# Optimization experiments

Hardware: AMD Instinct MI355X
Metric: run time of the kernel (lower is better)

## Reference

```python
import jax, jax.numpy as jnp
import numpy as np

N_NODES = 50000
N_EDGES = 1600000
N_CAND = 1000
N_GRAPHS = 50
EMB = 32
EDGE_DIM = 1
L = 4
EPS = 1e-5


def setup_inputs() -> dict:
    key = jax.random.key(0)
    ks = jax.random.split(key, 24)
    x = jax.random.normal(ks[0], (N_NODES, 2), dtype=jnp.float32)
    edge_index = jax.random.randint(ks[1], (2, N_EDGES), 0, N_NODES)
    edge_attr = jax.random.normal(ks[2], (N_EDGES, EDGE_DIM), dtype=jnp.float32)
    candidate_idxs = jax.random.randint(ks[3], (N_CAND,), 0, N_NODES)
    batch = jnp.sort(jax.random.randint(ks[4], (N_NODES,), 0, N_GRAPHS))
    s = 0.1
    W_in = jax.random.normal(ks[5], (2, EMB), dtype=jnp.float32) * s
    b_in = jax.random.normal(ks[6], (EMB,), dtype=jnp.float32) * s
    # stacked per-layer MLP params: Linear(65->32), BN, ReLU, Linear(32->32), BN, ReLU
    W1 = jax.random.normal(ks[7], (L, 2 * EMB + EDGE_DIM, EMB), dtype=jnp.float32) * s
    b1 = jax.random.normal(ks[8], (L, EMB), dtype=jnp.float32) * s
    g1 = 1.0 + 0.1 * jax.random.normal(ks[9], (L, EMB), dtype=jnp.float32)
    be1 = 0.1 * jax.random.normal(ks[10], (L, EMB), dtype=jnp.float32)
    m1 = 0.1 * jax.random.normal(ks[11], (L, EMB), dtype=jnp.float32)
    v1 = 0.5 + jax.random.uniform(ks[12], (L, EMB), dtype=jnp.float32)
    W2 = jax.random.normal(ks[13], (L, EMB, EMB), dtype=jnp.float32) * s
    b2 = jax.random.normal(ks[14], (L, EMB), dtype=jnp.float32) * s
    g2 = 1.0 + 0.1 * jax.random.normal(ks[15], (L, EMB), dtype=jnp.float32)
    be2 = 0.1 * jax.random.normal(ks[16], (L, EMB), dtype=jnp.float32)
    m2 = 0.1 * jax.random.normal(ks[17], (L, EMB), dtype=jnp.float32)
    v2 = 0.5 + jax.random.uniform(ks[18], (L, EMB), dtype=jnp.float32)
    W_out = jax.random.normal(ks[19], (EMB, 1), dtype=jnp.float32) * s
    b_out = jax.random.normal(ks[20], (1,), dtype=jnp.float32) * s
    return dict(x=x, edge_index=edge_index, edge_attr=edge_attr,
                candidate_idxs=candidate_idxs, batch=batch,
                W_in=W_in, b_in=b_in, W1=W1, b1=b1, g1=g1, be1=be1, m1=m1, v1=v1,
                W2=W2, b2=b2, g2=g2, be2=be2, m2=m2, v2=v2, W_out=W_out, b_out=b_out)


def _bn(h, g, b, m, v):
    # eval-mode BatchNorm1d
    return (h - m) * (g * jax.lax.rsqrt(v + EPS)) + b


def _forward(x, edge_index, edge_attr, candidate_idxs, batch,
             W_in, b_in, W1, b1, g1, be1, m1, v1,
             W2, b2, g2, be2, m2, v2, W_out, b_out):
    src = edge_index[0]  # x_j
    dst = edge_index[1]  # x_i (aggregation target)
    h = x @ W_in + b_in  # [N, EMB]

    def layer(h, p):
        (w1, bb1, gg1, bbe1, mm1, vv1, w2, bb2, gg2, bbe2, mm2, vv2) = p
        msg = jnp.concatenate([h[dst], h[src], edge_attr], axis=-1)  # [E, 2*EMB+edge_dim]
        t = jax.nn.relu(_bn(msg @ w1 + bb1, gg1, bbe1, mm1, vv1))
        t = jax.nn.relu(_bn(t @ w2 + bb2, gg2, bbe2, mm2, vv2))
        agg = jax.ops.segment_sum(t, dst, num_segments=N_NODES)
        return h + agg, None

    h, _ = jax.lax.scan(layer, h, (W1, b1, g1, be1, m1, v1, W2, b2, g2, be2, m2, v2))

    logits = (h[candidate_idxs] @ W_out + b_out).squeeze(-1)  # [C]
    seg = batch[candidate_idxs]
    seg_max = jax.ops.segment_max(logits, seg, num_segments=N_GRAPHS)
    z = logits - seg_max[seg]
    lse = jnp.log(jax.ops.segment_sum(jnp.exp(z), seg, num_segments=N_GRAPHS))
    return z - lse[seg]


def reference(x, edge_index, edge_attr, candidate_idxs, batch,
              W_in, b_in, W1, b1, g1, be1, m1, v1,
              W2, b2, g2, be2, m2, v2, W_out, b_out):
    return _forward(x, edge_index, edge_attr, candidate_idxs, batch,
                    W_in, b_in, W1, b1, g1, be1, m1, v1,
                    W2, b2, g2, be2, m2, v2, W_out, b_out)
```

## Files before the change

kernel.cpp:

```cpp
#include <hip/hip_runtime.h>
#include <hip/hip_bf16.h>

#define N_NODES 50000
#define N_EDGES 1600000
#define N_CAND  1000
#define N_GRAPHS 50
#define EMB 32
#define L_LAYERS 4

#define BSH 8
#define BNODES 256
#define NBK ((N_NODES + BNODES - 1) >> BSH)
#define STILE 2048
#define NBLK_S ((N_EDGES + STILE - 1) / STILE)

#define NPW 8

#define W1A_OFF 0
#define W1B_OFF 4096
#define W2_OFF  8192
#define WE_OFF  12288
#define C1_OFF  12416
#define C2_OFF  12544
#define W2H_OFF  12672
#define WEH_OFF  14720
#define W1AH_OFF 14784
#define W1BH_OFF 16832
#define H_OFF    18880
#define NODE_F  (N_NODES * EMB)

#define BH_OFF    (H_OFF + 4 * NODE_F)
#define BOFF_OFF  (BH_OFF + NBK)
#define OFFS_OFF  (BOFF_OFF + NBK + 1)
#define CSR_OFF   (OFFS_OFF + N_NODES + 1)
#define T_OFF     (CSR_OFF + N_EDGES)

typedef float f32x4 __attribute__((ext_vector_type(4)));
typedef _Float16 f16x8 __attribute__((ext_vector_type(8)));

union HU { unsigned short u; _Float16 f; };
static __device__ __forceinline__ _Float16 h16(unsigned short u) { HU c; c.u = u; return c.f; }
static __device__ __forceinline__ unsigned short u16(_Float16 f) { HU c; c.f = f; return c.u; }

__global__ void prep_k(const float* __restrict__ W1, const float* __restrict__ b1,
                       const float* __restrict__ g1, const float* __restrict__ be1,
                       const float* __restrict__ m1, const float* __restrict__ v1,
                       const float* __restrict__ W2, const float* __restrict__ b2,
                       const float* __restrict__ g2, const float* __restrict__ be2,
                       const float* __restrict__ m2, const float* __restrict__ v2,
                       float* __restrict__ ws) {
    int t = threadIdx.x;
    _Float16* W2H  = (_Float16*)(ws + W2H_OFF);
    _Float16* WEH  = (_Float16*)(ws + WEH_OFF);
    _Float16* W1AH = (_Float16*)(ws + W1AH_OFF);
    _Float16* W1BH = (_Float16*)(ws + W1BH_OFF);
    for (int l = 0; l < L_LAYERS; ++l) {
        for (int i = t; i < 1024; i += 256) {
            int k = i >> 5, j = i & 31;
            float s1 = g1[l * 32 + j] * rsqrtf(v1[l * 32 + j] + 1e-5f);
            float s2 = g2[l * 32 + j] * rsqrtf(v2[l * 32 + j] + 1e-5f);
            float wa = W1[(l * 65 + k) * 32 + j] * s1;
            float wb = W1[(l * 65 + 32 + k) * 32 + j] * s1;
            ws[W1A_OFF + l * 1024 + i] = wa;
            ws[W1B_OFF + l * 1024 + i] = wb;
            W1AH[l * 1024 + i] = (_Float16)wa;
            W1BH[l * 1024 + i] = (_Float16)wb;
            float w2v = W2[(l * 32 + k) * 32 + j] * s2;
            ws[W2_OFF + l * 1024 + i] = w2v;
            W2H[l * 1024 + i] = (_Float16)w2v;
            if (k == 0) {
                float wev = W1[(l * 65 + 64) * 32 + j] * s1;
                ws[WE_OFF + l * 32 + j] = wev;
                WEH[l * 32 + j] = (_Float16)wev;
                ws[C1_OFF + l * 32 + j] = b1[l * 32 + j] * s1 + be1[l * 32 + j] - m1[l * 32 + j] * s1;
                ws[C2_OFF + l * 32 + j] = b2[l * 32 + j] * s2 + be2[l * 32 + j] - m2[l * 32 + j] * s2;
            }
        }
    }
}

__global__ void embed_node_k(const float* __restrict__ x, const float* __restrict__ Win,
                             const float* __restrict__ bin, const float* __restrict__ ws,
                             float* __restrict__ h, _Float16* __restrict__ hA,
                             _Float16* __restrict__ hB) {
    __shared__ float sA[1024], sB[1024];
    for (int i = threadIdx.x; i < 1024; i += blockDim.x) {
        sA[i] = ws[W1A_OFF + i];
        sB[i] = ws[W1B_OFF + i];
    }
    __syncthreads();
    int t = blockIdx.x * blockDim.x + threadIdx.x;
    if (t >= NODE_F) return;
    int n = t >> 5, j = t & 31;
    float hv = x[2 * n] * Win[j] + x[2 * n + 1] * Win[32 + j] + bin[j];
    h[t] = hv;
    float a = ws[C1_OFF + j];
    float b = 0.f;
#pragma unroll
    for (int k = 0; k < 32; ++k) {
        float hk = __shfl(hv, k, 32);
        a += hk * sA[k * 32 + j];
        b += hk * sB[k * 32 + j];
    }
    hA[t] = (_Float16)a;
    hB[t] = (_Float16)b;
}

__global__ void zero_k(int* __restrict__ p, int n) {
    int t = blockIdx.x * blockDim.x + threadIdx.x;
    if (t < n) p[t] = 0;
}

__global__ void bhist_k(const int* __restrict__ ei, int* __restrict__ bh, int* __restrict__ T) {
    __shared__ int lh[NBK];
    for (int i = threadIdx.x; i < NBK; i += 512) lh[i] = 0;
    __syncthreads();
    int tb = blockIdx.x * STILE;
#pragma unroll
    for (int i = 0; i < STILE / 512; ++i) {
        int e = tb + i * 512 + threadIdx.x;
        if (e < N_EDGES) atomicAdd(&lh[ei[N_EDGES + e] >> BSH], 1);
    }
    __syncthreads();
    for (int i = threadIdx.x; i < NBK; i += 512) {
        int c = lh[i];
        T[i * NBLK_S + blockIdx.x] = c;
        if (c) atomicAdd(&bh[i], c);
    }
}

__global__ void bscan_k(const int* __restrict__ bh, int* __restrict__ boffs) {
    __shared__ int part[1024];
    int t = threadIdx.x;
    int s = (t < NBK) ? bh[t] : 0;
    part[t] = s;
    __syncthreads();
    for (int d = 1; d < 1024; d <<= 1) {
        int v = (t >= d) ? part[t - d] : 0;
        __syncthreads();
        part[t] += v;
        __syncthreads();
    }
    if (t < NBK) boffs[t] = part[t] - s;
    if (t == 1023) boffs[NBK] = N_EDGES;
}

__global__ void bcursor_k(const int* __restrict__ boffs, int* __restrict__ T) {
    __shared__ int part[1024];
    int k = blockIdx.x, t = threadIdx.x;
    int v = (t < NBLK_S) ? T[k * NBLK_S + t] : 0;
    part[t] = v;
    __syncthreads();
    for (int d = 1; d < 1024; d <<= 1) {
        int u = (t >= d) ? part[t - d] : 0;
        __syncthreads();
        part[t] += u;
        __syncthreads();
    }
    if (t < NBLK_S) T[k * NBLK_S + t] = boffs[k] + part[t] - v;
}

__global__ void bscatter_k(const int* __restrict__ ei, const float* __restrict__ ea,
                           const int* __restrict__ T, int* __restrict__ stage_e,
                           unsigned char* __restrict__ stage_d) {
    __shared__ int lofs[NBK];
    for (int i = threadIdx.x; i < NBK; i += 512)
        lofs[i] = T[i * NBLK_S + blockIdx.x];
    __syncthreads();
    int tb = blockIdx.x * STILE;
#pragma unroll
    for (int i = 0; i < STILE / 512; ++i) {
        int e = tb + i * 512 + threadIdx.x;
        if (e < N_EDGES) {
            int src = ei[e], dst = ei[N_EDGES + e];
            int bk = dst >> BSH;
            int pos = atomicAdd(&lofs[bk], 1);
            unsigned short eh = u16((_Float16)ea[e]);
            stage_e[pos] = src | ((int)eh << 16);
            stage_d[pos] = (unsigned char)(dst & (BNODES - 1));
        }
    }
}

__global__ void bsort2_k(const int* __restrict__ boffs, const int* __restrict__ stage_e,
                         const unsigned char* __restrict__ stage_d,
                         int* __restrict__ offs, int* __restrict__ csr) {
    __shared__ int cnt[BNODES];
    __shared__ int pre[BNODES];
    __shared__ int cur[BNODES];
    const int b = blockIdx.x;
    const int nbase = b << BSH;
    const int t = threadIdx.x;
    const int beg = boffs[b], end = boffs[b + 1];
    if (t < BNODES) cnt[t] = 0;
    __syncthreads();
    for (int i = beg + t; i < end; i += 512)
        atomicAdd(&cnt[stage_d[i]], 1);
    __syncthreads();
    if (t < 64) {
        int b4 = t * 4;
        int c0 = cnt[b4], c1 = cnt[b4 + 1], c2 = cnt[b4 + 2], c3 = cnt[b4 + 3];
        int s = c0 + c1 + c2 + c3;
        int run = s;
#pragma unroll
        for (int d = 1; d < 64; d <<= 1) {
            int v = __shfl_up(run, d, 64);
            if (t >= d) run += v;
        }
        int ex = run - s;
        pre[b4] = ex; pre[b4 + 1] = ex + c0; pre[b4 + 2] = ex + c0 + c1; pre[b4 + 3] = ex + c0 + c1 + c2;
    }
    __syncthreads();
    if (t < BNODES) {
        cur[t] = pre[t];
        int n = nbase + t;
        if (n < N_NODES) offs[n] = beg + pre[t];
    }
    if (b == NBK - 1 && t == 0) offs[N_NODES] = N_EDGES;
    __syncthreads();
    for (int i = beg + t; i < end; i += 512) {
        int dloc = stage_d[i];
        int pos = beg + atomicAdd(&cur[dloc], 1);
        csr[pos] = stage_e[i];
    }
}

__launch_bounds__(256, 4)
__global__ void edge_mfma_k(const int* __restrict__ offs, const int* __restrict__ csr,
                            const float* __restrict__ ws, int l,
                            const float* __restrict__ h, const _Float16* __restrict__ hA,
                            const _Float16* __restrict__ hB, float* __restrict__ hnext,
                            _Float16* __restrict__ hAout, _Float16* __restrict__ hBout,
                            int doNext) {
    __shared__ float vbuf[4 * 256];
    const int lane = threadIdx.x & 63;
    const int wid = (blockIdx.x * 256 + threadIdx.x) >> 6;
    const int r = lane & 15;
    const int q = lane >> 4;
    const int ll = lane & 31;
    float* vb = vbuf + (threadIdx.x >> 6) * 256;
    const int nbase = wid * NPW;
    if (nbase >= N_NODES) return;

    int o[NPW + 1];
#pragma unroll
    for (int i = 0; i <= NPW; ++i)
        o[i] = __builtin_amdgcn_readfirstlane(offs[nbase + i]);

    const _Float16* W2H = (const _Float16*)(ws + W2H_OFF);
    f16x8 b0, b1;
#pragma unroll
    for (int i = 0; i < 8; ++i) {
        b0[i] = W2H[l * 1024 + (8 * q + i) * 32 + r];
        b1[i] = W2H[l * 1024 + (8 * q + i) * 32 + 16 + r];
    }
    const float c2a = ws[C2_OFF + l * 32 + r];
    const float c2b = ws[C2_OFF + l * 32 + 16 + r];
    const f32x4 zc0 = {c2a, c2a, c2a, c2a};
    const f32x4 zc1 = {c2b, c2b, c2b, c2b};
    const f16x8 we = *(const f16x8*)((const _Float16*)(ws + WEH_OFF) + l * 32 + 8 * q);
    const f16x8 zero8 = {};

#define CEI(EB, LIM) ({ int _e = (EB) + r; _e = (_e < (LIM)) ? _e : (LIM); _e = (_e > 0) ? _e : 0; _e; })

    int lim[NPW];
#pragma unroll
    for (int s = 0; s < NPW; ++s) {
        int e1 = o[s + 1] - 1;
        lim[s] = (e1 > 0) ? e1 : 0;
    }
    int pc[NPW], pn[NPW];
#pragma unroll
    for (int s = 0; s < NPW; ++s) pc[s] = csr[CEI(o[s], lim[s])];
    f16x8 hc[NPW];
#pragma unroll
    for (int s = 0; s < NPW; ++s)
        hc[s] = *(const f16x8*)(hB + (pc[s] & 0xFFFF) * 32 + 8 * q);
#pragma unroll
    for (int s = 0; s < NPW; ++s) pn[s] = csr[CEI(o[s] + 16, lim[s])];

#pragma unroll
    for (int p = 0; p < 4; ++p) {
        const int s0 = 2 * p, s1 = 2 * p + 1;
        const int n0 = nbase + s0;
        const int n1 = n0 + 1;
        const int o0 = o[s0], o1 = o[s1], o2 = o[s1 + 1];

        const f16x8 hA0 = *(const f16x8*)(hA + n0 * 32 + 8 * q);
        const f16x8 hA1 = *(const f16x8*)(hA + n1 * 32 + 8 * q);

        float ns00 = 0.f, ns01 = 0.f, ns10 = 0.f, ns11 = 0.f;
        int nit = (o1 - o0 + 15) >> 4;
        int nit1 = (o2 - o1 + 15) >> 4;
        if (nit1 > nit) nit = nit1;

        if (nit > 0) {
            const int lim0 = lim[s0], lim1 = lim[s1];
            int eb0 = o0, eb1 = o1;
            int pc0 = pc[s0], pc1 = pc[s1];
            f16x8 hc0 = hc[s0], hc1 = hc[s1];
            int pn0 = pn[s0], pn1 = pn[s1];
            for (int it = 0; it < nit; ++it) {
                f16x8 hn0 = *(const f16x8*)(hB + (pn0 & 0xFFFF) * 32 + 8 * q);
                f16x8 hn1 = *(const f16x8*)(hB + (pn1 & 0xFFFF) * 32 + 8 * q);
                int pm0 = csr[CEI(eb0 + 32, lim0)];
                int pm1 = csr[CEI(eb1 + 32, lim1)];
                _Float16 eah0 = h16((unsigned short)((unsigned)pc0 >> 16));
                _Float16 eah1 = h16((unsigned short)((unsigned)pc1 >> 16));
                f16x8 a0 = __builtin_elementwise_max(we * eah0 + (hA0 + hc0), zero8);
                f16x8 a1 = __builtin_elementwise_max(we * eah1 + (hA1 + hc1), zero8);
                f32x4 acc00 = __builtin_amdgcn_mfma_f32_16x16x32_f16(a0, b0, zc0, 0, 0, 0);
                f32x4 acc01 = __builtin_amdgcn_mfma_f32_16x16x32_f16(a0, b1, zc1, 0, 0, 0);
                f32x4 acc10 = __builtin_amdgcn_mfma_f32_16x16x32_f16(a1, b0, zc0, 0, 0, 0);
                f32x4 acc11 = __builtin_amdgcn_mfma_f32_16x16x32_f16(a1, b1, zc1, 0, 0, 0);
                int nr0 = o1 - eb0;
                int nr1 = o2 - eb1;
#pragma unroll
                for (int reg = 0; reg < 4; ++reg) {
                    int row = 4 * q + reg;
                    float m0 = (row < nr0) ? 1.f : 0.f;
                    float m1 = (row < nr1) ? 1.f : 0.f;
                    ns00 = fmaf(m0, fmaxf(acc00[reg], 0.f), ns00);
                    ns01 = fmaf(m0, fmaxf(acc01[reg], 0.f), ns01);
                    ns10 = fmaf(m1, fmaxf(acc10[reg], 0.f), ns10);
                    ns11 = fmaf(m1, fmaxf(acc11[reg], 0.f), ns11);
                }
                eb0 += 16; eb1 += 16;
                pc0 = pn0; pc1 = pn1;
                hc0 = hn0; hc1 = hn1;
                pn0 = pm0; pn1 = pm1;
            }
        }
        ns00 += __shfl_xor(ns00, 16, 64);
        ns00 += __shfl_xor(ns00, 32, 64);
        ns01 += __shfl_xor(ns01, 16, 64);
        ns01 += __shfl_xor(ns01, 32, 64);
        ns10 += __shfl_xor(ns10, 16, 64);
        ns10 += __shfl_xor(ns10, 32, 64);
        ns11 += __shfl_xor(ns11, 16, 64);
        ns11 += __shfl_xor(ns11, 32, 64);

        float v;
        if (lane < 32) {
            v = h[n0 * 32 + ll] + ((ll & 16) ? ns01 : ns00);
            hnext[n0 * 32 + ll] = v;
        } else {
            v = h[n1 * 32 + ll] + ((ll & 16) ? ns11 : ns10);
            hnext[n1 * 32 + ll] = v;
        }
        int node8 = s0 + (lane >> 5);
        vb[node8 * 32 + (ll ^ (node8 << 2))] = v;
    }
#undef CEI

    if (doNext) {
        const int lw = l + 1;
        f16x8 av;
#pragma unroll
        for (int i = 0; i < 8; ++i) {
            int rr = r & 7;
            int ch = 8 * q + i;
            float vv = vb[rr * 32 + (ch ^ (rr << 2))];
            av[i] = (r < 8) ? (_Float16)vv : (_Float16)0.f;
        }
        const _Float16* W1AH = (const _Float16*)(ws + W1AH_OFF) + lw * 1024;
        const _Float16* W1BH = (const _Float16*)(ws + W1BH_OFF) + lw * 1024;
        f16x8 wa0, wa1, wb0, wb1;
#pragma unroll
        for (int i = 0; i < 8; ++i) {
            wa0[i] = W1AH[(8 * q + i) * 32 + r];
            wa1[i] = W1AH[(8 * q + i) * 32 + 16 + r];
            wb0[i] = W1BH[(8 * q + i) * 32 + r];
            wb1[i] = W1BH[(8 * q + i) * 32 + 16 + r];
        }
        const float c1a = ws[C1_OFF + lw * 32 + r];
        const float c1b = ws[C1_OFF + lw * 32 + 16 + r];
        const f32x4 ca = {c1a, c1a, c1a, c1a};
        const f32x4 cb = {c1b, c1b, c1b, c1b};
        const f32x4 z4 = {0.f, 0.f, 0.f, 0.f};
        f32x4 dA0 = __builtin_amdgcn_mfma_f32_16x16x32_f16(av, wa0, ca, 0, 0, 0);
        f32x4 dA1 = __builtin_amdgcn_mfma_f32_16x16x32_f16(av, wa1, cb, 0, 0, 0);
        f32x4 dB0 = __builtin_amdgcn_mfma_f32_16x16x32_f16(av, wb0, z4, 0, 0, 0);
        f32x4 dB1 = __builtin_amdgcn_mfma_f32_16x16x32_f16(av, wb1, z4, 0, 0, 0);
#pragma unroll
        for (int reg = 0; reg < 4; ++reg) {
            int row = 4 * q + reg;
            int n = nbase + row;
            if (row < 8 && n < N_NODES) {
                hAout[n * 32 + r]      = (_Float16)dA0[reg];
                hAout[n * 32 + 16 + r] = (_Float16)dA1[reg];
                hBout[n * 32 + r]      = (_Float16)dB0[reg];
                hBout[n * 32 + 16 + r] = (_Float16)dB1[reg];
            }
        }
    }
}

__global__ void head_k(const float* __restrict__ h, const int* __restrict__ cand,
                       const int* __restrict__ batch, const float* __restrict__ Wout,
                       const float* __restrict__ bout, float* __restrict__ out) {
    __shared__ float Lg[N_CAND];
    __shared__ int Sg[N_CAND];
    __shared__ float gm[N_GRAPHS], gs[N_GRAPHS];
    int t = threadIdx.x;
    if (t < N_CAND) {
        int c = cand[t];
        float acc = bout[0];
#pragma unroll
        for (int j = 0; j < 32; ++j) acc += h[c * 32 + j] * Wout[j];
        Lg[t] = acc;
        Sg[t] = batch[c];
    }
    __syncthreads();
    if (t < 16 * N_GRAPHS) {
        int g = t >> 4, s = t & 15;
        float m = -1e30f;
        for (int i = s; i < N_CAND; i += 16)
            if (Sg[i] == g) m = fmaxf(m, Lg[i]);
#pragma unroll
        for (int d = 1; d < 16; d <<= 1) m = fmaxf(m, __shfl_xor(m, d, 64));
        float ssum = 0.f;
        for (int i = s; i < N_CAND; i += 16)
            if (Sg[i] == g) ssum += expf(Lg[i] - m);
#pragma unroll
        for (int d = 1; d < 16; d <<= 1) ssum += __shfl_xor(ssum, d, 64);
        if (s == 0) { gm[g] = m; gs[g] = logf(ssum); }
    }
    __syncthreads();
    if (t < N_CAND) out[t] = Lg[t] - gm[Sg[t]] - gs[Sg[t]];
}

extern "C" void kernel_launch(void* const* d_in, const int* in_sizes, int n_in,
                              void* d_out, int out_size, void* d_ws, size_t ws_size,
                              hipStream_t stream) {
    const float* x    = (const float*)d_in[0];
    const int*   ei   = (const int*)d_in[1];
    const float* eatt = (const float*)d_in[2];
    const int*   cand = (const int*)d_in[3];
    const int*   batch= (const int*)d_in[4];
    const float* Win  = (const float*)d_in[5];
    const float* bin  = (const float*)d_in[6];
    const float* W1   = (const float*)d_in[7];
    const float* b1   = (const float*)d_in[8];
    const float* g1   = (const float*)d_in[9];
    const float* be1  = (const float*)d_in[10];
    const float* m1   = (const float*)d_in[11];
    const float* v1   = (const float*)d_in[12];
    const float* W2   = (const float*)d_in[13];
    const float* b2   = (const float*)d_in[14];
    const float* g2   = (const float*)d_in[15];
    const float* be2  = (const float*)d_in[16];
    const float* m2   = (const float*)d_in[17];
    const float* v2   = (const float*)d_in[18];
    const float* Wout = (const float*)d_in[19];
    const float* bout = (const float*)d_in[20];
    float* out = (float*)d_out;
    float* ws = (float*)d_ws;

    float* h0 = ws + H_OFF;
    float* h1 = ws + H_OFF + NODE_F;
    _Float16* hA0 = (_Float16*)(ws + H_OFF + 2 * NODE_F);
    _Float16* hB0 = (_Float16*)(ws + H_OFF + 2 * NODE_F + NODE_F / 2);
    _Float16* hA1 = (_Float16*)(ws + H_OFF + 3 * NODE_F);
    _Float16* hB1 = (_Float16*)(ws + H_OFF + 3 * NODE_F + NODE_F / 2);
    int* bh    = (int*)(ws + BH_OFF);
    int* boffs = (int*)(ws + BOFF_OFF);
    int* offs  = (int*)(ws + OFFS_OFF);
    int* csr   = (int*)(ws + CSR_OFF);
    int* T     = (int*)(ws + T_OFF);
    int* stage_e = (int*)(ws + H_OFF + NODE_F);
    unsigned char* stage_d = (unsigned char*)(ws + H_OFF + 2 * NODE_F);

    prep_k<<<1, 256, 0, stream>>>(W1, b1, g1, be1, m1, v1, W2, b2, g2, be2, m2, v2, ws);

    zero_k<<<(NBK + 255) / 256, 256, 0, stream>>>(bh, NBK);
    bhist_k<<<NBLK_S, 512, 0, stream>>>(ei, bh, T);
    bscan_k<<<1, 1024, 0, stream>>>(bh, boffs);
    bcursor_k<<<NBK, 1024, 0, stream>>>(boffs, T);
    bscatter_k<<<NBLK_S, 512, 0, stream>>>(ei, eatt, T, stage_e, stage_d);
    bsort2_k<<<NBK, 512, 0, stream>>>(boffs, stage_e, stage_d, offs, csr);

    embed_node_k<<<(NODE_F + 1023) / 1024, 1024, 0, stream>>>(x, Win, bin, ws, h0, hA0, hB0);

    const int waves = (N_NODES + NPW - 1) / NPW;
    const int eblocks = (waves + 3) / 4;
    float* cur = h0;
    float* nxt = h1;
    _Float16 *cA = hA0, *cB = hB0, *nA = hA1, *nB = hB1;
    for (int l = 0; l < L_LAYERS; ++l) {
        edge_mfma_k<<<eblocks, 256, 0, stream>>>(offs, csr, ws, l, cur, cA, cB,
                                                 nxt, nA, nB, l < L_LAYERS - 1);
        float* tf = cur; cur = nxt; nxt = tf;
        _Float16* t1 = cA; cA = nA; nA = t1;
        _Float16* t2 = cB; cB = nB; nB = t2;
    }

    head_k<<<1, 1024, 0, stream>>>(cur, cand, batch, Wout, bout, out);
}
```

Measured before the change: 242.4 us.

## Halve nodes per wave, shuffle-based next-layer staging, pack sort stage into int2

```diff
diff --git a/kernel.cpp b/kernel.cpp
--- a/kernel.cpp
+++ b/kernel.cpp
@@ -14,7 +14,7 @@
 #define STILE 2048
 #define NBLK_S ((N_EDGES + STILE - 1) / STILE)
 
-#define NPW 8
+#define NPW 4
 
 #define W1A_OFF 0
 #define W1B_OFF 4096
@@ -161,8 +161,7 @@
 }
 
 __global__ void bscatter_k(const int* __restrict__ ei, const float* __restrict__ ea,
-                           const int* __restrict__ T, int* __restrict__ stage_e,
-                           unsigned char* __restrict__ stage_d) {
+                           const int* __restrict__ T, int2* __restrict__ stage) {
     __shared__ int lofs[NBK];
     for (int i = threadIdx.x; i < NBK; i += 512)
         lofs[i] = T[i * NBLK_S + blockIdx.x];
@@ -175,15 +174,15 @@
             int src = ei[e], dst = ei[N_EDGES + e];
             int bk = dst >> BSH;
             int pos = atomicAdd(&lofs[bk], 1);
-            unsigned short eh = u16((_Float16)ea[e]);
-            stage_e[pos] = src | ((int)eh << 16);
-            stage_d[pos] = (unsigned char)(dst & (BNODES - 1));
-        }
-    }
-}
-
-__global__ void bsort2_k(const int* __restrict__ boffs, const int* __restrict__ stage_e,
-                         const unsigned char* __restrict__ stage_d,
+            int2 p;
+            p.x = src | ((dst & (BNODES - 1)) << 16);
+            p.y = __float_as_int(ea[e]);
+            stage[pos] = p;
+        }
+    }
+}
+
+__global__ void bsort2_k(const int* __restrict__ boffs, const int2* __restrict__ stage,
                          int* __restrict__ offs, int* __restrict__ csr) {
     __shared__ int cnt[BNODES];
     __shared__ int pre[BNODES];
@@ -195,7 +194,7 @@
     if (t < BNODES) cnt[t] = 0;
     __syncthreads();
     for (int i = beg + t; i < end; i += 512)
-        atomicAdd(&cnt[stage_d[i]], 1);
+        atomicAdd(&cnt[(stage[i].x >> 16) & (BNODES - 1)], 1);
     __syncthreads();
     if (t < 64) {
         int b4 = t * 4;
@@ -219,26 +218,26 @@
     if (b == NBK - 1 && t == 0) offs[N_NODES] = N_EDGES;
     __syncthreads();
     for (int i = beg + t; i < end; i += 512) {
-        int dloc = stage_d[i];
+        int2 p = stage[i];
+        int dloc = (p.x >> 16) & (BNODES - 1);
         int pos = beg + atomicAdd(&cur[dloc], 1);
-        csr[pos] = stage_e[i];
-    }
-}
-
-__launch_bounds__(256, 4)
+        unsigned short eh = u16((_Float16)__int_as_float(p.y));
+        csr[pos] = (p.x & 0xFFFF) | ((int)eh << 16);
+    }
+}
+
+__launch_bounds__(256, 6)
 __global__ void edge_mfma_k(const int* __restrict__ offs, const int* __restrict__ csr,
                             const float* __restrict__ ws, int l,
                             const float* __restrict__ h, const _Float16* __restrict__ hA,
                             const _Float16* __restrict__ hB, float* __restrict__ hnext,
                             _Float16* __restrict__ hAout, _Float16* __restrict__ hBout,
                             int doNext) {
-    __shared__ float vbuf[4 * 256];
     const int lane = threadIdx.x & 63;
     const int wid = (blockIdx.x * 256 + threadIdx.x) >> 6;
     const int r = lane & 15;
     const int q = lane >> 4;
     const int ll = lane & 31;
-    float* vb = vbuf + (threadIdx.x >> 6) * 256;
     const int nbase = wid * NPW;
     if (nbase >= N_NODES) return;
 
@@ -279,8 +278,10 @@
 #pragma unroll
     for (int s = 0; s < NPW; ++s) pn[s] = csr[CEI(o[s] + 16, lim[s])];
 
-#pragma unroll
-    for (int p = 0; p < 4; ++p) {
+    float vsave[2];
+
+#pragma unroll
+    for (int p = 0; p < 2; ++p) {
         const int s0 = 2 * p, s1 = 2 * p + 1;
         const int n0 = nbase + s0;
         const int n1 = n0 + 1;
@@ -348,20 +349,20 @@
             v = h[n1 * 32 + ll] + ((ll & 16) ? ns11 : ns10);
             hnext[n1 * 32 + ll] = v;
         }
-        int node8 = s0 + (lane >> 5);
-        vb[node8 * 32 + (ll ^ (node8 << 2))] = v;
+        vsave[p] = v;
     }
 #undef CEI
 
     if (doNext) {
         const int lw = l + 1;
+        const int srcb = ((r & 1) << 5);
         f16x8 av;
 #pragma unroll
         for (int i = 0; i < 8; ++i) {
-            int rr = r & 7;
-            int ch = 8 * q + i;
-            float vv = vb[rr * 32 + (ch ^ (rr << 2))];
-            av[i] = (r < 8) ? (_Float16)vv : (_Float16)0.f;
+            int src = srcb + 8 * q + i;
+            float a0 = __shfl(vsave[0], src, 64);
+            float a1 = __shfl(vsave[1], src, 64);
+            av[i] = (_Float16)((r & 2) ? a1 : a0);
         }
         const _Float16* W1AH = (const _Float16*)(ws + W1AH_OFF) + lw * 1024;
         const _Float16* W1BH = (const _Float16*)(ws + W1BH_OFF) + lw * 1024;
@@ -386,7 +387,7 @@
         for (int reg = 0; reg < 4; ++reg) {
             int row = 4 * q + reg;
             int n = nbase + row;
-            if (row < 8 && n < N_NODES) {
+            if (row < NPW) {
                 hAout[n * 32 + r]      = (_Float16)dA0[reg];
                 hAout[n * 32 + 16 + r] = (_Float16)dA1[reg];
                 hBout[n * 32 + r]      = (_Float16)dB0[reg];
@@ -468,8 +469,7 @@
     int* offs  = (int*)(ws + OFFS_OFF);
     int* csr   = (int*)(ws + CSR_OFF);
     int* T     = (int*)(ws + T_OFF);
-    int* stage_e = (int*)(ws + H_OFF + NODE_F);
-    unsigned char* stage_d = (unsigned char*)(ws + H_OFF + 2 * NODE_F);
+    int2* stage = (int2*)(ws + H_OFF + NODE_F);
 
     prep_k<<<1, 256, 0, stream>>>(W1, b1, g1, be1, m1, v1, W2, b2, g2, be2, m2, v2, ws);
 
@@ -477,8 +477,8 @@
     bhist_k<<<NBLK_S, 512, 0, stream>>>(ei, bh, T);
     bscan_k<<<1, 1024, 0, stream>>>(bh, boffs);
     bcursor_k<<<NBK, 1024, 0, stream>>>(boffs, T);
-    bscatter_k<<<NBLK_S, 512, 0, stream>>>(ei, eatt, T, stage_e, stage_d);
-    bsort2_k<<<NBK, 512, 0, stream>>>(boffs, stage_e, stage_d, offs, csr);
+    bscatter_k<<<NBLK_S, 512, 0, stream>>>(ei, eatt, T, stage);
+    bsort2_k<<<NBK, 512, 0, stream>>>(boffs, stage, offs, csr);
 
     embed_node_k<<<(NODE_F + 1023) / 1024, 1024, 0, stream>>>(x, Win, bin, ws, h0, hA0, hB0);
 
```

Result: slower. 252.4 us (+4.2%).
